# Kernel tuning notes

Measured on AMD Instinct MI355X. Metric: run time of the kernel, lower is better.

Reference implementation:

```python
import jax, jax.numpy as jnp
import numpy as np

D_IN = 768
D_MODEL = 768
NUM_HEADS = 12
DEPTH = D_MODEL // NUM_HEADS


def setup_inputs() -> dict:
    key = jax.random.key(0)
    ks = jax.random.split(key, 9)
    B, N = 2, 2048
    s_in = 1.0 / np.sqrt(D_IN)
    s_md = 1.0 / np.sqrt(D_MODEL)
    return {
        "x": jax.random.normal(ks[0], (B, N, D_IN), dtype=jnp.float32),
        "wq": jax.random.normal(ks[1], (D_IN, D_MODEL), dtype=jnp.float32) * s_in,
        "bq": jax.random.normal(ks[2], (D_MODEL,), dtype=jnp.float32) * 0.02,
        "wk": jax.random.normal(ks[3], (D_IN, D_MODEL), dtype=jnp.float32) * s_in,
        "bk": jax.random.normal(ks[4], (D_MODEL,), dtype=jnp.float32) * 0.02,
        "wv": jax.random.normal(ks[5], (D_IN, D_MODEL), dtype=jnp.float32) * s_in,
        "bv": jax.random.normal(ks[6], (D_MODEL,), dtype=jnp.float32) * 0.02,
        "wo": jax.random.normal(ks[7], (D_MODEL, D_MODEL), dtype=jnp.float32) * s_md,
        "bo": jax.random.normal(ks[8], (D_MODEL,), dtype=jnp.float32) * 0.02,
    }


def reference(x, wq, bq, wk, bk, wv, bv, wo, bo):
    B, N, _ = x.shape
    H, D = NUM_HEADS, DEPTH
    # project and split heads: [B,N,H,D] -> [B,H,N,D]
    q = (x @ wq + bq).reshape(B, N, H, D).transpose(0, 2, 1, 3)
    k = (x @ wk + bk).reshape(B, N, H, D).transpose(0, 2, 1, 3)
    v = (x @ wv + bv).reshape(B, N, H, D).transpose(0, 2, 1, 3)
    scale = 1.0 / jnp.sqrt(jnp.asarray(D, dtype=q.dtype))
    attn = jnp.einsum('bhnd,bhmd->bhnm', q, k) * scale  # [B,H,N,N]
    attn = jax.nn.softmax(attn, axis=-1)
    z = jnp.einsum('bhnm,bhmd->bhnd', attn, v)
    z = z.transpose(0, 2, 1, 3).reshape(B, N, H * D)
    return z @ wo + bo
```

## Files before the change

kernel.cpp:

```cpp
#include <hip/hip_runtime.h>
#include <hip/hip_bf16.h>
#include <math.h>

#define NH 12
#define DH 64
#define BB 2
#define NN 2048
#define DM 768

typedef short v8s __attribute__((ext_vector_type(8)));
typedef float v4f __attribute__((ext_vector_type(4)));

__device__ __forceinline__ unsigned short f2bf(float f) {
    union { float f; unsigned u; } x; x.f = f;
    unsigned r = x.u + 0x7fffu + ((x.u >> 16) & 1u);
    return (unsigned short)(r >> 16);
}

__device__ __forceinline__ int cvtpk(float lo, float hi2) {
    int r;
    asm("v_cvt_pk_bf16_f32 %0, %1, %2" : "=v"(r) : "v"(lo), "v"(hi2));
    return r;
}

__device__ __forceinline__ void glds16(const void* g, void* l) {
    __builtin_amdgcn_global_load_lds((const __attribute__((address_space(1))) void*)g,
                                     (__attribute__((address_space(3))) void*)l, 16, 0, 0);
}

__global__ __launch_bounds__(256) void cast_x_k(const float* __restrict__ in,
                                                unsigned short* __restrict__ out, int n) {
    int i = (blockIdx.x * 256 + threadIdx.x) * 4;
    if (i >= n) return;
    float4 v = *(const float4*)(in + i);
    ushort4 o;
    o.x = f2bf(v.x); o.y = f2bf(v.y); o.z = f2bf(v.z); o.w = f2bf(v.w);
    *(ushort4*)(out + i) = o;
}

__global__ __launch_bounds__(256) void cast_wT_k(const float* __restrict__ w0, const float* __restrict__ w1,
                                                 const float* __restrict__ w2, const float* __restrict__ w3,
                                                 unsigned short* __restrict__ o0, unsigned short* __restrict__ o1,
                                                 unsigned short* __restrict__ o2, unsigned short* __restrict__ o3) {
    __shared__ unsigned short t[64][65];
    const float* in; unsigned short* out;
    switch (blockIdx.y) {
        case 0: in = w0; out = o0; break;
        case 1: in = w1; out = o1; break;
        case 2: in = w2; out = o2; break;
        default: in = w3; out = o3; break;
    }
    int kt = blockIdx.x / 12, ct = blockIdx.x % 12;
    int rr = threadIdx.x >> 4, cc = threadIdx.x & 15;
#pragma unroll
    for (int it = 0; it < 4; it++) {
        int row = kt * 64 + it * 16 + rr;
        int col = ct * 64 + cc * 4;
        float4 v = *(const float4*)(in + row * 768 + col);
        t[it * 16 + rr][cc * 4 + 0] = f2bf(v.x);
        t[it * 16 + rr][cc * 4 + 1] = f2bf(v.y);
        t[it * 16 + rr][cc * 4 + 2] = f2bf(v.z);
        t[it * 16 + rr][cc * 4 + 3] = f2bf(v.w);
    }
    __syncthreads();
#pragma unroll
    for (int it = 0; it < 4; it++) {
        int c_l = it * 16 + rr;
        int k_l = cc * 4;
        ushort4 o;
        o.x = t[k_l + 0][c_l];
        o.y = t[k_l + 1][c_l];
        o.z = t[k_l + 2][c_l];
        o.w = t[k_l + 3][c_l];
        *(ushort4*)(out + (ct * 64 + c_l) * 768 + kt * 64 + k_l) = o;
    }
}

__global__ __launch_bounds__(256) void qkv_gemm_k(
    const unsigned short* __restrict__ xb,
    const unsigned short* __restrict__ wqT, const unsigned short* __restrict__ wkT,
    const unsigned short* __restrict__ wvT,
    const float* __restrict__ bq, const float* __restrict__ bk, const float* __restrict__ bv,
    unsigned short* __restrict__ q, unsigned short* __restrict__ k, unsigned short* __restrict__ vT) {
    __shared__ unsigned short Abuf[3][128 * 32];
    __shared__ unsigned short Bbuf[3][128 * 32];

    int ctile = blockIdx.x;
    int mtile = blockIdx.y;
    int mat = ctile / 6;
    int col0 = (ctile % 6) * 128;
    const unsigned short* Bsrc = (mat == 0) ? wqT : ((mat == 1) ? wkT : wvT);
    const float* bias = (mat == 0) ? bq : ((mat == 1) ? bk : bv);

    int tid = threadIdx.x;
    int w = tid >> 6, l = tid & 63;
    int q16 = l & 15, g = l >> 4;
    int wr = w >> 1, wc = w & 1;

    int srow0 = tid >> 2;
    int ss = tid & 3;

    auto stage = [&](int tt, int buf) {
        int k0 = tt * 32;
#pragma unroll
        for (int i = 0; i < 2; ++i) {
            int row = srow0 + i * 64;
            int c16 = ss ^ ((row >> 1) & 3);
            glds16(xb + (mtile * 128 + row) * 768 + k0 + (c16 << 3),
                   (char*)&Abuf[buf][0] + i * 4096 + tid * 16);
            glds16(Bsrc + (col0 + row) * 768 + k0 + (c16 << 3),
                   (char*)&Bbuf[buf][0] + i * 4096 + tid * 16);
        }
    };

    v4f zero = {0.f, 0.f, 0.f, 0.f};
    v4f acc[4][4];
#pragma unroll
    for (int i = 0; i < 4; i++)
#pragma unroll
        for (int j = 0; j < 4; j++) acc[i][j] = zero;

    stage(0, 0);
    stage(1, 1);
    asm volatile("s_waitcnt vmcnt(4)" ::: "memory");
    __builtin_amdgcn_s_barrier();
    asm volatile("" ::: "memory");

    int rd = 0;
    for (int tt = 0; tt < 24; ++tt) {
        int st = rd + 2; if (st >= 3) st -= 3;
        if (tt + 2 < 24) stage(tt + 2, st);
        const char* Ab = (const char*)&Abuf[rd][0];
        const char* Bb = (const char*)&Bbuf[rd][0];
        v8s af[4], bf[4];
#pragma unroll
        for (int f = 0; f < 4; f++) {
            int arow = wr * 64 + f * 16 + q16;
            af[f] = *(const v8s*)(Ab + arow * 64 + ((g ^ ((arow >> 1) & 3)) << 4));
            int brow = wc * 64 + f * 16 + q16;
            bf[f] = *(const v8s*)(Bb + brow * 64 + ((g ^ ((brow >> 1) & 3)) << 4));
        }
#pragma unroll
        for (int i = 0; i < 4; i++)
#pragma unroll
            for (int j = 0; j < 4; j++)
                acc[i][j] = __builtin_amdgcn_mfma_f32_16x16x32_bf16(af[i], bf[j], acc[i][j], 0, 0, 0);
        asm volatile("s_waitcnt vmcnt(4)" ::: "memory");
        __builtin_amdgcn_s_barrier();
        asm volatile("" ::: "memory");
        rd = (rd + 1 == 3) ? 0 : rd + 1;
    }

    const float QSCL = 0.125f * 1.44269504088896340736f;
#pragma unroll
    for (int i = 0; i < 4; i++)
#pragma unroll
        for (int j = 0; j < 4; j++)
#pragma unroll
            for (int r = 0; r < 4; r++) {
                int gr = mtile * 128 + wr * 64 + i * 16 + 4 * g + r;
                int gcl = col0 + wc * 64 + j * 16 + q16;
                int b = gr / NN, n = gr % NN;
                int h = gcl / DH, d = gcl % DH;
                int bh = b * NH + h;
                float v = acc[i][j][r] + bias[gcl];
                if (mat == 0)      q[(bh * NN + n) * DH + d]  = f2bf(v * QSCL);
                else if (mat == 1) k[(bh * NN + n) * DH + d]  = f2bf(v);
                else               vT[(bh * DH + d) * NN + n] = f2bf(v);
            }
}

__global__ __launch_bounds__(512) void attn_k(
    const unsigned short* __restrict__ q, const unsigned short* __restrict__ k,
    const unsigned short* __restrict__ vT, unsigned short* __restrict__ z) {
    __shared__ __align__(16) char Kb[2][2][4096];
    __shared__ __align__(16) char Vb[2][2][4096];
    __shared__ unsigned short plds[8][16][36];

    int bh = blockIdx.x % 24;
    int qt = blockIdx.x / 24;
    int b = bh / NH, h = bh % NH;
    int tid = threadIdx.x;
    int w = tid >> 6, l = tid & 63;
    int q16 = l & 15, g = l >> 4;
    int ws = w & 3, hf = w >> 2;

    const unsigned short* qp = q + (size_t)bh * NN * DH;
    const unsigned short* kp = k + (size_t)bh * NN * DH;
    const unsigned short* vp = vT + (size_t)bh * DH * NN;
    int qrow = qt * 64 + ws * 16 + q16;

    v8s qf0 = *(const v8s*)(qp + qrow * DH + 8 * g);
    v8s qf1 = *(const v8s*)(qp + qrow * DH + 32 + 8 * g);

    v8s ones;
#pragma unroll
    for (int i = 0; i < 8; i++) ones[i] = (short)0x3F80;

    int hf_s = tid >> 8;
    int s8 = tid & 255;
    int krow_s = s8 >> 3, ksl = s8 & 7;
    int kc16 = ksl ^ (krow_s & 7);
    int vrow_s = s8 >> 2, vsl = s8 & 3;
    int vc16 = vsl ^ (vrow_s & 3);

    auto stage = [&](int t, int buf) {
        int kv0 = hf_s * (NN / 2) + t * 32;
        glds16(kp + (kv0 + krow_s) * DH + (kc16 << 3), &Kb[hf_s][buf][s8 * 16]);
        glds16(vp + (size_t)vrow_s * NN + kv0 + (vc16 << 3), &Vb[hf_s][buf][s8 * 16]);
    };

    v4f zero = {0.f, 0.f, 0.f, 0.f};
    float mrow = -INFINITY;
    v4f o[4];
    v4f osum = zero;
#pragma unroll
    for (int dt = 0; dt < 4; dt++) o[dt] = zero;

    stage(0, 0);
    __syncthreads();

    for (int t = 0; t < 32; ++t) {
        int cur = t & 1;
        if (t + 1 < 32) stage(t + 1, cur ^ 1);

        const char* kb = &Kb[hf][cur][0];
        const char* vb = &Vb[hf][cur][0];

        v4f st[2];
#pragma unroll
        for (int ct = 0; ct < 2; ct++) {
            int krow = ct * 16 + q16;
            v8s kf0 = *(const v8s*)(kb + krow * 128 + ((g ^ (krow & 7)) << 4));
            v8s kf1 = *(const v8s*)(kb + krow * 128 + (((4 + g) ^ (krow & 7)) << 4));
            st[ct] = __builtin_amdgcn_mfma_f32_16x16x32_bf16(kf0, qf0, zero, 0, 0, 0);
            st[ct] = __builtin_amdgcn_mfma_f32_16x16x32_bf16(kf1, qf1, st[ct], 0, 0, 0);
        }

        float ma = fmaxf(fmaxf(st[0][0], st[0][1]), st[0][2]);
        float mb = fmaxf(fmaxf(st[0][3], st[1][0]), st[1][1]);
        float vmax = fmaxf(fmaxf(ma, mb), fmaxf(st[1][2], st[1][3]));
        vmax = fmaxf(vmax, __shfl_xor(vmax, 16));
        vmax = fmaxf(vmax, __shfl_xor(vmax, 32));

        if (!__all(vmax <= mrow + 8.f)) {
            float mn = fmaxf(mrow, vmax);
            float sc = exp2f(mrow - mn);
#pragma unroll
            for (int dt = 0; dt < 4; dt++)
#pragma unroll
                for (int r = 0; r < 4; r++) o[dt][r] *= sc;
            osum[0] *= sc;
            mrow = mn;
        }

#pragma unroll
        for (int ct = 0; ct < 2; ct++) {
            float p0 = exp2f(st[ct][0] - mrow);
            float p1 = exp2f(st[ct][1] - mrow);
            float p2 = exp2f(st[ct][2] - mrow);
            float p3 = exp2f(st[ct][3] - mrow);
            union { int i[2]; short4 s; } u;
            u.i[0] = cvtpk(p0, p1);
            u.i[1] = cvtpk(p2, p3);
            *(short4*)(&plds[w][q16][ct * 16 + 4 * g]) = u.s;
        }

        v8s pf0 = *(const v8s*)(&plds[w][q16][8 * g]);

        osum = __builtin_amdgcn_mfma_f32_16x16x32_bf16(ones, pf0, osum, 0, 0, 0);

#pragma unroll
        for (int dt = 0; dt < 4; dt++) {
            int dcol = dt * 16 + q16;
            v8s vf = *(const v8s*)(vb + dcol * 64 + ((g ^ (dcol & 3)) << 4));
            o[dt] = __builtin_amdgcn_mfma_f32_16x16x32_bf16(vf, pf0, o[dt], 0, 0, 0);
        }
        __syncthreads();
    }

    float* po = (float*)&Kb[0][0][0];
    float* pm = (float*)&Vb[0][0][0];
    float* pl = pm + 64;
    int row = ws * 16 + q16;

    if (hf == 1) {
#pragma unroll
        for (int dt = 0; dt < 4; dt++)
#pragma unroll
            for (int r = 0; r < 4; r++)
                po[row * 64 + dt * 16 + 4 * g + r] = o[dt][r];
        if (g == 0) { pm[row] = mrow; pl[row] = osum[0]; }
    }
    __syncthreads();
    if (hf == 0) {
        float m1 = pm[row], l1 = pl[row];
        float ms = fmaxf(mrow, m1);
        float a0 = exp2f(mrow - ms), a1 = exp2f(m1 - ms);
        float inv = 1.f / (osum[0] * a0 + l1 * a1);
        int n = qt * 64 + ws * 16 + q16;
#pragma unroll
        for (int dt = 0; dt < 4; dt++) {
            short4 s4;
            s4.x = (short)f2bf((o[dt][0] * a0 + po[row * 64 + dt * 16 + 4 * g + 0] * a1) * inv);
            s4.y = (short)f2bf((o[dt][1] * a0 + po[row * 64 + dt * 16 + 4 * g + 1] * a1) * inv);
            s4.z = (short)f2bf((o[dt][2] * a0 + po[row * 64 + dt * 16 + 4 * g + 2] * a1) * inv);
            s4.w = (short)f2bf((o[dt][3] * a0 + po[row * 64 + dt * 16 + 4 * g + 3] * a1) * inv);
            *(short4*)(&z[((size_t)(b * NN + n)) * DM + h * DH + dt * 16 + 4 * g]) = s4;
        }
    }
}

__global__ __launch_bounds__(256) void out_gemm_k(
    const unsigned short* __restrict__ zb, const unsigned short* __restrict__ woT,
    const float* __restrict__ bo, float* __restrict__ out) {
    __shared__ unsigned short Abuf[3][128 * 32];
    __shared__ unsigned short Bbuf[3][128 * 32];

    int ctile = blockIdx.x;
    int mtile = blockIdx.y;
    int col0 = ctile * 128;

    int tid = threadIdx.x;
    int w = tid >> 6, l = tid & 63;
    int q16 = l & 15, g = l >> 4;
    int wr = w >> 1, wc = w & 1;

    int srow0 = tid >> 2;
    int ss = tid & 3;

    auto stage = [&](int tt, int buf) {
        int k0 = tt * 32;
#pragma unroll
        for (int i = 0; i < 2; ++i) {
            int row = srow0 + i * 64;
            int c16 = ss ^ ((row >> 1) & 3);
            glds16(zb + (mtile * 128 + row) * 768 + k0 + (c16 << 3),
                   (char*)&Abuf[buf][0] + i * 4096 + tid * 16);
            glds16(woT + (col0 + row) * 768 + k0 + (c16 << 3),
                   (char*)&Bbuf[buf][0] + i * 4096 + tid * 16);
        }
    };

    v4f zero = {0.f, 0.f, 0.f, 0.f};
    v4f acc[4][4];
#pragma unroll
    for (int i = 0; i < 4; i++)
#pragma unroll
        for (int j = 0; j < 4; j++) acc[i][j] = zero;

    stage(0, 0);
    stage(1, 1);
    asm volatile("s_waitcnt vmcnt(4)" ::: "memory");
    __builtin_amdgcn_s_barrier();
    asm volatile("" ::: "memory");

    int rd = 0;
    for (int tt = 0; tt < 24; ++tt) {
        int st = rd + 2; if (st >= 3) st -= 3;
        if (tt + 2 < 24) stage(tt + 2, st);
        const char* Ab = (const char*)&Abuf[rd][0];
        const char* Bb = (const char*)&Bbuf[rd][0];
        v8s af[4], bf[4];
#pragma unroll
        for (int f = 0; f < 4; f++) {
            int arow = wr * 64 + f * 16 + q16;
            af[f] = *(const v8s*)(Ab + arow * 64 + ((g ^ ((arow >> 1) & 3)) << 4));
            int brow = wc * 64 + f * 16 + q16;
            bf[f] = *(const v8s*)(Bb + brow * 64 + ((g ^ ((brow >> 1) & 3)) << 4));
        }
#pragma unroll
        for (int i = 0; i < 4; i++)
#pragma unroll
            for (int j = 0; j < 4; j++)
                acc[i][j] = __builtin_amdgcn_mfma_f32_16x16x32_bf16(af[i], bf[j], acc[i][j], 0, 0, 0);
        asm volatile("s_waitcnt vmcnt(4)" ::: "memory");
        __builtin_amdgcn_s_barrier();
        asm volatile("" ::: "memory");
        rd = (rd + 1 == 3) ? 0 : rd + 1;
    }

#pragma unroll
    for (int i = 0; i < 4; i++)
#pragma unroll
        for (int j = 0; j < 4; j++)
#pragma unroll
            for (int r = 0; r < 4; r++) {
                int gr = mtile * 128 + wr * 64 + i * 16 + 4 * g + r;
                int gc = col0 + wc * 64 + j * 16 + q16;
                out[gr * 768 + gc] = acc[i][j][r] + bo[gc];
            }
}

extern "C" void kernel_launch(void* const* d_in, const int* in_sizes, int n_in,
                              void* d_out, int out_size, void* d_ws, size_t ws_size,
                              hipStream_t stream) {
    const float* x  = (const float*)d_in[0];
    const float* wq = (const float*)d_in[1];
    const float* bq = (const float*)d_in[2];
    const float* wk = (const float*)d_in[3];
    const float* bk = (const float*)d_in[4];
    const float* wv = (const float*)d_in[5];
    const float* bv = (const float*)d_in[6];
    const float* wo = (const float*)d_in[7];
    const float* bo = (const float*)d_in[8];
    float* out = (float*)d_out;

    const int NX = BB * NN * DM;
    const int NW = 768 * 768;

    unsigned short* wsp = (unsigned short*)d_ws;
    unsigned short* xb  = wsp;
    unsigned short* wqT = xb + NX;
    unsigned short* wkT = wqT + NW;
    unsigned short* wvT = wkT + NW;
    unsigned short* woT = wvT + NW;
    unsigned short* qb  = woT + NW;
    unsigned short* kb  = qb + NX;
    unsigned short* vTb = kb + NX;
    unsigned short* zb  = vTb + NX;

    cast_x_k<<<NX / (256 * 4), 256, 0, stream>>>(x, xb, NX);
    cast_wT_k<<<dim3(144, 4), 256, 0, stream>>>(wq, wk, wv, wo, wqT, wkT, wvT, woT);
    qkv_gemm_k<<<dim3(18, 32), 256, 0, stream>>>(xb, wqT, wkT, wvT, bq, bk, bv, qb, kb, vTb);
    attn_k<<<BB * NH * (NN / 64), 512, 0, stream>>>(qb, kb, vTb, zb);
    out_gemm_k<<<dim3(6, 32), 256, 0, stream>>>(zb, woT, bo, out);
}
```

Baseline: 125.0 us.

## Use 8-wave GEMM blocks and re-swizzle V tile LDS layout in attention

Both projection GEMMs now launch 512 threads per 128x128 tile, so each wave computes a 64x32 sub-tile with half the accumulators, and each thread stages one 16-byte chunk per matrix instead of two. The aim is more waves in flight for latency hiding on the small grids (576 and 192 blocks). The attention kernel's V tile staging is reorganised to 128-byte rows with an 8-way XOR swizzle, meant to reduce LDS bank conflicts on the V fragment reads. In exchange, the A and B fragments are re-read from LDS by more waves per block.

```diff
diff --git a/kernel.cpp b/kernel.cpp
--- a/kernel.cpp
+++ b/kernel.cpp
@@ -76,7 +76,7 @@
     }
 }
 
-__global__ __launch_bounds__(256) void qkv_gemm_k(
+__global__ __launch_bounds__(512) void qkv_gemm_k(
     const unsigned short* __restrict__ xb,
     const unsigned short* __restrict__ wqT, const unsigned short* __restrict__ wkT,
     const unsigned short* __restrict__ wvT,
@@ -95,34 +95,30 @@
     int tid = threadIdx.x;
     int w = tid >> 6, l = tid & 63;
     int q16 = l & 15, g = l >> 4;
-    int wr = w >> 1, wc = w & 1;
-
-    int srow0 = tid >> 2;
+    int wr = w >> 2, wc = w & 3;
+
+    int srow = tid >> 2;
     int ss = tid & 3;
+    int c16s = ss ^ ((srow >> 1) & 3);
 
     auto stage = [&](int tt, int buf) {
         int k0 = tt * 32;
-#pragma unroll
-        for (int i = 0; i < 2; ++i) {
-            int row = srow0 + i * 64;
-            int c16 = ss ^ ((row >> 1) & 3);
-            glds16(xb + (mtile * 128 + row) * 768 + k0 + (c16 << 3),
-                   (char*)&Abuf[buf][0] + i * 4096 + tid * 16);
-            glds16(Bsrc + (col0 + row) * 768 + k0 + (c16 << 3),
-                   (char*)&Bbuf[buf][0] + i * 4096 + tid * 16);
-        }
+        glds16(xb + (mtile * 128 + srow) * 768 + k0 + (c16s << 3),
+               (char*)&Abuf[buf][0] + tid * 16);
+        glds16(Bsrc + (col0 + srow) * 768 + k0 + (c16s << 3),
+               (char*)&Bbuf[buf][0] + tid * 16);
     };
 
     v4f zero = {0.f, 0.f, 0.f, 0.f};
-    v4f acc[4][4];
+    v4f acc[4][2];
 #pragma unroll
     for (int i = 0; i < 4; i++)
 #pragma unroll
-        for (int j = 0; j < 4; j++) acc[i][j] = zero;
+        for (int j = 0; j < 2; j++) acc[i][j] = zero;
 
     stage(0, 0);
     stage(1, 1);
-    asm volatile("s_waitcnt vmcnt(4)" ::: "memory");
+    asm volatile("s_waitcnt vmcnt(2)" ::: "memory");
     __builtin_amdgcn_s_barrier();
     asm volatile("" ::: "memory");
 
@@ -132,20 +128,23 @@
         if (tt + 2 < 24) stage(tt + 2, st);
         const char* Ab = (const char*)&Abuf[rd][0];
         const char* Bb = (const char*)&Bbuf[rd][0];
-        v8s af[4], bf[4];
+        v8s af[4], bf[2];
 #pragma unroll
         for (int f = 0; f < 4; f++) {
             int arow = wr * 64 + f * 16 + q16;
             af[f] = *(const v8s*)(Ab + arow * 64 + ((g ^ ((arow >> 1) & 3)) << 4));
-            int brow = wc * 64 + f * 16 + q16;
-            bf[f] = *(const v8s*)(Bb + brow * 64 + ((g ^ ((brow >> 1) & 3)) << 4));
+        }
+#pragma unroll
+        for (int j = 0; j < 2; j++) {
+            int brow = wc * 32 + j * 16 + q16;
+            bf[j] = *(const v8s*)(Bb + brow * 64 + ((g ^ ((brow >> 1) & 3)) << 4));
         }
 #pragma unroll
         for (int i = 0; i < 4; i++)
 #pragma unroll
-            for (int j = 0; j < 4; j++)
+            for (int j = 0; j < 2; j++)
                 acc[i][j] = __builtin_amdgcn_mfma_f32_16x16x32_bf16(af[i], bf[j], acc[i][j], 0, 0, 0);
-        asm volatile("s_waitcnt vmcnt(4)" ::: "memory");
+        asm volatile("s_waitcnt vmcnt(2)" ::: "memory");
         __builtin_amdgcn_s_barrier();
         asm volatile("" ::: "memory");
         rd = (rd + 1 == 3) ? 0 : rd + 1;
@@ -155,11 +154,11 @@
 #pragma unroll
     for (int i = 0; i < 4; i++)
 #pragma unroll
-        for (int j = 0; j < 4; j++)
+        for (int j = 0; j < 2; j++)
 #pragma unroll
             for (int r = 0; r < 4; r++) {
                 int gr = mtile * 128 + wr * 64 + i * 16 + 4 * g + r;
-                int gcl = col0 + wc * 64 + j * 16 + q16;
+                int gcl = col0 + wc * 32 + j * 16 + q16;
                 int b = gr / NN, n = gr % NN;
                 int h = gcl / DH, d = gcl % DH;
                 int bh = b * NH + h;
@@ -199,15 +198,16 @@
 
     int hf_s = tid >> 8;
     int s8 = tid & 255;
-    int krow_s = s8 >> 3, ksl = s8 & 7;
-    int kc16 = ksl ^ (krow_s & 7);
-    int vrow_s = s8 >> 2, vsl = s8 & 3;
-    int vc16 = vsl ^ (vrow_s & 3);
+    int row_s = s8 >> 3, sl = s8 & 7;
+    int kc16 = (sl ^ (row_s & 7)) & 7;
+    int vj = sl ^ (row_s & 7);
+    int vd = row_s + ((vj >> 2) << 5);
+    int vkw = vj & 3;
 
     auto stage = [&](int t, int buf) {
         int kv0 = hf_s * (NN / 2) + t * 32;
-        glds16(kp + (kv0 + krow_s) * DH + (kc16 << 3), &Kb[hf_s][buf][s8 * 16]);
-        glds16(vp + (size_t)vrow_s * NN + kv0 + (vc16 << 3), &Vb[hf_s][buf][s8 * 16]);
+        glds16(kp + (kv0 + row_s) * DH + (kc16 << 3), &Kb[hf_s][buf][s8 * 16]);
+        glds16(vp + (size_t)vd * NN + kv0 + vkw * 8, &Vb[hf_s][buf][s8 * 16]);
     };
 
     v4f zero = {0.f, 0.f, 0.f, 0.f};
@@ -273,7 +273,9 @@
 #pragma unroll
         for (int dt = 0; dt < 4; dt++) {
             int dcol = dt * 16 + q16;
-            v8s vf = *(const v8s*)(vb + dcol * 64 + ((g ^ (dcol & 3)) << 4));
+            int rr = dcol & 31;
+            int sl2 = (((dcol >> 5) << 2) + g) ^ (rr & 7);
+            v8s vf = *(const v8s*)(vb + rr * 128 + (sl2 << 4));
             o[dt] = __builtin_amdgcn_mfma_f32_16x16x32_bf16(vf, pf0, o[dt], 0, 0, 0);
         }
         __syncthreads();
@@ -311,7 +313,7 @@
     }
 }
 
-__global__ __launch_bounds__(256) void out_gemm_k(
+__global__ __launch_bounds__(512) void out_gemm_k(
     const unsigned short* __restrict__ zb, const unsigned short* __restrict__ woT,
     const float* __restrict__ bo, float* __restrict__ out) {
     __shared__ unsigned short Abuf[3][128 * 32];
@@ -324,34 +326,30 @@
     int tid = threadIdx.x;
     int w = tid >> 6, l = tid & 63;
     int q16 = l & 15, g = l >> 4;
-    int wr = w >> 1, wc = w & 1;
-
-    int srow0 = tid >> 2;
+    int wr = w >> 2, wc = w & 3;
+
+    int srow = tid >> 2;
     int ss = tid & 3;
+    int c16s = ss ^ ((srow >> 1) & 3);
 
     auto stage = [&](int tt, int buf) {
         int k0 = tt * 32;
-#pragma unroll
-        for (int i = 0; i < 2; ++i) {
-            int row = srow0 + i * 64;
-            int c16 = ss ^ ((row >> 1) & 3);
-            glds16(zb + (mtile * 128 + row) * 768 + k0 + (c16 << 3),
-                   (char*)&Abuf[buf][0] + i * 4096 + tid * 16);
-            glds16(woT + (col0 + row) * 768 + k0 + (c16 << 3),
-                   (char*)&Bbuf[buf][0] + i * 4096 + tid * 16);
-        }
+        glds16(zb + (mtile * 128 + srow) * 768 + k0 + (c16s << 3),
+               (char*)&Abuf[buf][0] + tid * 16);
+        glds16(woT + (col0 + srow) * 768 + k0 + (c16s << 3),
+               (char*)&Bbuf[buf][0] + tid * 16);
     };
 
     v4f zero = {0.f, 0.f, 0.f, 0.f};
-    v4f acc[4][4];
+    v4f acc[4][2];
 #pragma unroll
     for (int i = 0; i < 4; i++)
 #pragma unroll
-        for (int j = 0; j < 4; j++) acc[i][j] = zero;
+        for (int j = 0; j < 2; j++) acc[i][j] = zero;
 
     stage(0, 0);
     stage(1, 1);
-    asm volatile("s_waitcnt vmcnt(4)" ::: "memory");
+    asm volatile("s_waitcnt vmcnt(2)" ::: "memory");
     __builtin_amdgcn_s_barrier();
     asm volatile("" ::: "memory");
 
@@ -361,20 +359,23 @@
         if (tt + 2 < 24) stage(tt + 2, st);
         const char* Ab = (const char*)&Abuf[rd][0];
         const char* Bb = (const char*)&Bbuf[rd][0];
-        v8s af[4], bf[4];
+        v8s af[4], bf[2];
 #pragma unroll
         for (int f = 0; f < 4; f++) {
             int arow = wr * 64 + f * 16 + q16;
             af[f] = *(const v8s*)(Ab + arow * 64 + ((g ^ ((arow >> 1) & 3)) << 4));
-            int brow = wc * 64 + f * 16 + q16;
-            bf[f] = *(const v8s*)(Bb + brow * 64 + ((g ^ ((brow >> 1) & 3)) << 4));
+        }
+#pragma unroll
+        for (int j = 0; j < 2; j++) {
+            int brow = wc * 32 + j * 16 + q16;
+            bf[j] = *(const v8s*)(Bb + brow * 64 + ((g ^ ((brow >> 1) & 3)) << 4));
         }
 #pragma unroll
         for (int i = 0; i < 4; i++)
 #pragma unroll
-            for (int j = 0; j < 4; j++)
+            for (int j = 0; j < 2; j++)
                 acc[i][j] = __builtin_amdgcn_mfma_f32_16x16x32_bf16(af[i], bf[j], acc[i][j], 0, 0, 0);
-        asm volatile("s_waitcnt vmcnt(4)" ::: "memory");
+        asm volatile("s_waitcnt vmcnt(2)" ::: "memory");
         __builtin_amdgcn_s_barrier();
         asm volatile("" ::: "memory");
         rd = (rd + 1 == 3) ? 0 : rd + 1;
@@ -383,11 +384,11 @@
 #pragma unroll
     for (int i = 0; i < 4; i++)
 #pragma unroll
-        for (int j = 0; j < 4; j++)
+        for (int j = 0; j < 2; j++)
 #pragma unroll
             for (int r = 0; r < 4; r++) {
                 int gr = mtile * 128 + wr * 64 + i * 16 + 4 * g + r;
-                int gc = col0 + wc * 64 + j * 16 + q16;
+                int gc = col0 + wc * 32 + j * 16 + q16;
                 out[gr * 768 + gc] = acc[i][j][r] + bo[gc];
             }
 }
@@ -422,7 +423,7 @@
 
     cast_x_k<<<NX / (256 * 4), 256, 0, stream>>>(x, xb, NX);
     cast_wT_k<<<dim3(144, 4), 256, 0, stream>>>(wq, wk, wv, wo, wqT, wkT, wvT, woT);
-    qkv_gemm_k<<<dim3(18, 32), 256, 0, stream>>>(xb, wqT, wkT, wvT, bq, bk, bv, qb, kb, vTb);
+    qkv_gemm_k<<<dim3(18, 32), 512, 0, stream>>>(xb, wqT, wkT, wvT, bq, bk, bv, qb, kb, vTb);
     attn_k<<<BB * NH * (NN / 64), 512, 0, stream>>>(qb, kb, vTb, zb);
-    out_gemm_k<<<dim3(6, 32), 256, 0, stream>>>(zb, woT, bo, out);
-}
+    out_gemm_k<<<dim3(6, 32), 512, 0, stream>>>(zb, woT, bo, out);
+}
```

New measurement: 119.3 us. 1.05x faster.
